# Performance work log

Hardware: AMD Instinct MI355X
Metric: run time of the kernel (lower is better)

Reference implementation:

```python
import jax, jax.numpy as jnp
import numpy as np

B, H, S, E = 1024, 64, 1, 512


def setup_inputs() -> dict:
    key = jax.random.key(0)
    k1, k2, k3, k4, k5 = jax.random.split(key, 5)
    return {
        "others1": jax.random.normal(k1, (B, H, S, E), dtype=jnp.float32),
        "others2": jax.random.normal(k2, (B, H, S, E), dtype=jnp.float32),
        "others3": jax.random.normal(k3, (B, H, S, E), dtype=jnp.float32),
        "main": jax.random.normal(k4, (B, H, S, E), dtype=jnp.float32),
        "W": jax.random.normal(k5, (E, E), dtype=jnp.float32) * 0.02,
    }


def reference(others1, others2, others3, main, W):
    # mean over the 'other' modalities, then drop the seq dim (squeeze(2))
    mean = (others1 + others2 + others3) / 3.0  # (B,H,1,E)
    m = mean[:, :, 0, :]   # (B,H,E)
    q = main[:, :, 0, :]   # (B,H,E)
    # score = mean @ W @ main^T  -> (B,H,H)
    score = jnp.einsum('bhe,ef,bgf->bhg', m, W, q)
    attn = jax.nn.softmax(score, axis=-1)          # (B,H,H)
    context = jnp.einsum('bhg,bge->bhe', attn, q)  # (B,H,E)
    return context, attn
```

## Files before the change

kernel.cpp:

```cpp
#include <hip/hip_runtime.h>
#include <hip/hip_bf16.h>

typedef _Float16 half4_t __attribute__((ext_vector_type(4)));
typedef _Float16 half8_t __attribute__((ext_vector_type(8)));
typedef float    float4_t __attribute__((ext_vector_type(4)));

#define MFMA32(a, b, c) __builtin_amdgcn_mfma_f32_16x16x32_f16((a), (b), (c), 0, 0, 0)

constexpr int  Bb  = 1024;
constexpr long CTX = (long)Bb * 64 * 512;
constexpr int  SQP = 520;
constexpr int  QTP = 72;

__global__ void w_pack(const float* __restrict__ W, _Float16* __restrict__ W2) {
    const int t = blockIdx.x * 256 + threadIdx.x;
    const int lane = t & 63, grp = t >> 6;
    const int E = grp >> 4, c = grp & 15;
    const int r16 = lane & 15, q = lane >> 4;
    const float* src = W + (long)(E * 16 + r16) * 512 + c * 32 + q * 8;
    float4_t x = *(const float4_t*)(src);
    float4_t y = *(const float4_t*)(src + 4);
    half8_t h;
    h[0]=(_Float16)x[0]; h[1]=(_Float16)x[1]; h[2]=(_Float16)x[2]; h[3]=(_Float16)x[3];
    h[4]=(_Float16)y[0]; h[5]=(_Float16)y[1]; h[6]=(_Float16)y[2]; h[7]=(_Float16)y[3];
    *(half8_t*)(W2 + (long)t * 8) = h;
}

__global__ __launch_bounds__(512, 4)
void ovo_score(const float* __restrict__ o1, const float* __restrict__ o2,
               const float* __restrict__ o3, const float* __restrict__ qm,
               const _Float16* __restrict__ W2, float* __restrict__ out)
{
    __shared__ __align__(16) _Float16 sQ[64 * SQP];

    const int t = threadIdx.x, lane = t & 63, w = t >> 6;
    const int r16 = lane & 15, q = lane >> 4;
    const long base = (long)blockIdx.x * 64 * 512;
    const float4_t zf4 = {0.f, 0.f, 0.f, 0.f};

    {
        const int srow = t >> 3;
        const int sf   = (t & 7) * 4;
        const float* qsrc = qm + base + (long)srow * 512 + sf;
        _Float16*    qdst = &sQ[srow * SQP + sf];
        #pragma unroll
        for (int k = 0; k < 16; ++k) {
            float4_t v = *(const float4_t*)(qsrc + k * 32);
            half4_t h;
            h[0]=(_Float16)v[0]; h[1]=(_Float16)v[1]; h[2]=(_Float16)v[2]; h[3]=(_Float16)v[3];
            *(half4_t*)(qdst + k * 32) = h;
        }
    }
    __syncthreads();

    float4_t vacc[4][4];
    #pragma unroll
    for (int i = 0; i < 4; ++i)
        #pragma unroll
        for (int j = 0; j < 4; ++j) vacc[i][j] = zf4;

    #pragma unroll
    for (int c = 0; c < 16; ++c) {
        half8_t Aq[4], Bw[4];
        #pragma unroll
        for (int gt = 0; gt < 4; ++gt)
            Aq[gt] = *(const half8_t*)(&sQ[(gt * 16 + r16) * SQP + c * 32 + q * 8]);
        #pragma unroll
        for (int et = 0; et < 4; ++et)
            Bw[et] = *(const half8_t*)(W2 + (long)((w * 4 + et) * 16 + c) * 512 + lane * 8);
        #pragma unroll
        for (int gt = 0; gt < 4; ++gt)
            #pragma unroll
            for (int et = 0; et < 4; ++et)
                vacc[gt][et] = MFMA32(Aq[gt], Bw[et], vacc[gt][et]);
    }

    __syncthreads();
    #pragma unroll
    for (int gt = 0; gt < 4; ++gt)
        #pragma unroll
        for (int et = 0; et < 4; ++et)
            #pragma unroll
            for (int r = 0; r < 4; ++r)
                sQ[(gt * 16 + q * 4 + r) * SQP + w * 64 + et * 16 + r16] =
                    (_Float16)vacc[gt][et][r];
    __syncthreads();

    const int ht = w & 3, eh = w >> 2;
    const long abase = base + (long)(ht * 16 + r16) * 512 + eh * 256 + q * 8;
    const int esV = eh * 256 + q * 8;

    float4_t sacc[4];
    #pragma unroll
    for (int i = 0; i < 4; ++i) sacc[i] = zf4;

    float4_t a1A, b1A, a2A, b2A, a3A, b3A;
    float4_t a1B, b1B, a2B, b2B, a3B, b3B;

    #define SLOAD(S, c) do { \
        const long o_ = abase + (c) * 32; \
        a1##S = *(const float4_t*)(o1 + o_); b1##S = *(const float4_t*)(o1 + o_ + 4); \
        a2##S = *(const float4_t*)(o2 + o_); b2##S = *(const float4_t*)(o2 + o_ + 4); \
        a3##S = *(const float4_t*)(o3 + o_); b3##S = *(const float4_t*)(o3 + o_ + 4); \
    } while (0)

    #define SCOMP(S, c) do { \
        float4_t m0 = (a1##S + a2##S + a3##S) * (1.0f / 3.0f); \
        float4_t m1 = (b1##S + b2##S + b3##S) * (1.0f / 3.0f); \
        half8_t af; \
        af[0]=(_Float16)m0[0]; af[1]=(_Float16)m0[1]; af[2]=(_Float16)m0[2]; af[3]=(_Float16)m0[3]; \
        af[4]=(_Float16)m1[0]; af[5]=(_Float16)m1[1]; af[6]=(_Float16)m1[2]; af[7]=(_Float16)m1[3]; \
        _Pragma("unroll") \
        for (int gt = 0; gt < 4; ++gt) { \
            half8_t bf = *(const half8_t*)(&sQ[(gt * 16 + r16) * SQP + esV + (c) * 32]); \
            sacc[gt] = MFMA32(af, bf, sacc[gt]); \
        } \
    } while (0)

    SLOAD(A, 0);
    #pragma unroll
    for (int cc = 0; cc < 8; cc += 2) {
        SLOAD(B, cc + 1);
        SCOMP(A, cc);
        if (cc + 2 < 8) SLOAD(A, cc + 2);
        SCOMP(B, cc + 1);
    }

    __syncthreads();
    float* part = reinterpret_cast<float*>(sQ);
    if (w >= 4) {
        #pragma unroll
        for (int gt = 0; gt < 4; ++gt)
            *(float4_t*)(&part[(((w - 4) * 4 + gt) * 64 + lane) * 4]) = sacc[gt];
    }
    __syncthreads();
    if (w < 4) {
        #pragma unroll
        for (int gt = 0; gt < 4; ++gt)
            sacc[gt] += *(const float4_t*)(&part[((w * 4 + gt) * 64 + lane) * 4]);
        #pragma unroll
        for (int r = 0; r < 4; ++r) {
            float mx = fmaxf(fmaxf(sacc[0][r], sacc[1][r]), fmaxf(sacc[2][r], sacc[3][r]));
            mx = fmaxf(mx, __shfl_xor(mx, 1));
            mx = fmaxf(mx, __shfl_xor(mx, 2));
            mx = fmaxf(mx, __shfl_xor(mx, 4));
            mx = fmaxf(mx, __shfl_xor(mx, 8));
            float p0 = __expf(sacc[0][r] - mx), p1 = __expf(sacc[1][r] - mx);
            float p2 = __expf(sacc[2][r] - mx), p3 = __expf(sacc[3][r] - mx);
            float s = p0 + p1 + p2 + p3;
            s += __shfl_xor(s, 1); s += __shfl_xor(s, 2);
            s += __shfl_xor(s, 4); s += __shfl_xor(s, 8);
            const float inv = 1.0f / s;
            float* arow = out + CTX + ((long)blockIdx.x * 64 + w * 16 + q * 4 + r) * 64;
            arow[ 0 + r16] = p0 * inv;
            arow[16 + r16] = p1 * inv;
            arow[32 + r16] = p2 * inv;
            arow[48 + r16] = p3 * inv;
        }
    }
}

__global__ __launch_bounds__(256, 4)
void ovo_ctx(const float* __restrict__ qm, const float* __restrict__ out_attn,
             float* __restrict__ out)
{
    __shared__ __align__(16) _Float16 qT[2][64 * QTP];

    const int t = threadIdx.x, lane = t & 63, w = t >> 6;
    const int r16 = lane & 15, q = lane >> 4;
    const long b = blockIdx.x;
    const long base = b * 64 * 512;
    const float4_t zf4 = {0.f, 0.f, 0.f, 0.f};

    const float* ap = out_attn + (b * 64 + w * 16 + r16) * 64 + q * 8;
    half8_t pA0, pA1;
    {
        float4_t x = *(const float4_t*)(ap + 0),  y = *(const float4_t*)(ap + 4);
        pA0[0]=(_Float16)x[0]; pA0[1]=(_Float16)x[1]; pA0[2]=(_Float16)x[2]; pA0[3]=(_Float16)x[3];
        pA0[4]=(_Float16)y[0]; pA0[5]=(_Float16)y[1]; pA0[6]=(_Float16)y[2]; pA0[7]=(_Float16)y[3];
        float4_t z = *(const float4_t*)(ap + 32), u = *(const float4_t*)(ap + 36);
        pA1[0]=(_Float16)z[0]; pA1[1]=(_Float16)z[1]; pA1[2]=(_Float16)z[2]; pA1[3]=(_Float16)z[3];
        pA1[4]=(_Float16)u[0]; pA1[5]=(_Float16)u[1]; pA1[6]=(_Float16)u[2]; pA1[7]=(_Float16)u[3];
    }

    const int sg = t & 63, se = (t >> 6) * 16;
    const float* qsrc = qm + base + (long)sg * 512 + se;
    float4_t rA[4], rB[4];

    #define QLOAD(R, c) do { \
        _Pragma("unroll") \
        for (int i = 0; i < 4; ++i) R[i] = *(const float4_t*)(qsrc + (c) * 64 + i * 4); \
    } while (0)
    #define QCOMMIT(R, buf) do { \
        _Pragma("unroll") \
        for (int i = 0; i < 4; ++i) \
            _Pragma("unroll") \
            for (int jj = 0; jj < 4; ++jj) \
                qT[buf][(se + i * 4 + jj) * QTP + sg] = (_Float16)R[i][jj]; \
    } while (0)

    #define BCOMP(c, buf) do { \
        _Pragma("unroll") \
        for (int et = 0; et < 4; ++et) { \
            half8_t b0 = *(const half8_t*)(&qT[buf][(et * 16 + r16) * QTP + q * 8]); \
            half8_t b1 = *(const half8_t*)(&qT[buf][(et * 16 + r16) * QTP + 32 + q * 8]); \
            float4_t acc = MFMA32(pA0, b0, zf4); \
            acc = MFMA32(pA1, b1, acc); \
            _Pragma("unroll") \
            for (int rr = 0; rr < 4; ++rr) \
                out[(b * 64 + w * 16 + q * 4 + rr) * 512 + (c) * 64 + et * 16 + r16] = acc[rr]; \
        } \
    } while (0)

    QLOAD(rA, 0);
    QCOMMIT(rA, 0);
    __syncthreads();
    #pragma unroll
    for (int cc = 0; cc < 8; cc += 2) {
        QLOAD(rB, cc + 1);
        BCOMP(cc, 0);
        QCOMMIT(rB, 1);
        __syncthreads();
        if (cc + 2 < 8) QLOAD(rA, cc + 2);
        BCOMP(cc + 1, 1);
        if (cc + 2 < 8) QCOMMIT(rA, 0);
        __syncthreads();
    }
}

extern "C" void kernel_launch(void* const* d_in, const int* in_sizes, int n_in,
                              void* d_out, int out_size, void* d_ws, size_t ws_size,
                              hipStream_t stream) {
    const float* o1 = (const float*)d_in[0];
    const float* o2 = (const float*)d_in[1];
    const float* o3 = (const float*)d_in[2];
    const float* qm = (const float*)d_in[3];
    const float* W  = (const float*)d_in[4];
    float* out = (float*)d_out;
    _Float16* W2 = (_Float16*)d_ws;

    w_pack<<<dim3(128), dim3(256), 0, stream>>>(W, W2);
    ovo_score<<<dim3(Bb), dim3(512), 0, stream>>>(o1, o2, o3, qm, W2, out);
    ovo_ctx<<<dim3(Bb), dim3(256), 0, stream>>>(qm, out + CTX, out);
}
```

Measured before the change: 211.6 us.

## Stage mean rows through double-buffered LDS with coalesced loads overlapping score MFMAs

The score kernel now loads the three 'other' tensors with fully coalesced contiguous float4 reads into registers, averages them and commits 16-row fp16 chunks into a double-buffered LDS tile (sM). Prefetch of the next chunk is overlapped with the MFMA work on the current chunk. The score tile is then staged through LDS so each softmax row can be handled with contiguous reads and vectorised row writes. This adds LDS usage and register pressure (launch bounds lowered to 2 blocks per CU), trading occupancy for better memory coalescing and overlap.

```diff
diff --git a/kernel.cpp b/kernel.cpp
--- a/kernel.cpp
+++ b/kernel.cpp
@@ -10,6 +10,8 @@
 constexpr int  Bb  = 1024;
 constexpr long CTX = (long)Bb * 64 * 512;
 constexpr int  SQP = 520;
+constexpr int  SMP = 520;
+constexpr int  SP  = 65;
 constexpr int  QTP = 72;
 
 __global__ void w_pack(const float* __restrict__ W, _Float16* __restrict__ W2) {
@@ -26,31 +28,47 @@
     *(half8_t*)(W2 + (long)t * 8) = h;
 }
 
-__global__ __launch_bounds__(512, 4)
+__global__ __launch_bounds__(512, 2)
 void ovo_score(const float* __restrict__ o1, const float* __restrict__ o2,
                const float* __restrict__ o3, const float* __restrict__ qm,
                const _Float16* __restrict__ W2, float* __restrict__ out)
 {
     __shared__ __align__(16) _Float16 sQ[64 * SQP];
+    __shared__ __align__(16) _Float16 sM[2][16 * SMP];
 
     const int t = threadIdx.x, lane = t & 63, w = t >> 6;
     const int r16 = lane & 15, q = lane >> 4;
+    const int gt = w & 3, eh = w >> 2;
     const long base = (long)blockIdx.x * 64 * 512;
     const float4_t zf4 = {0.f, 0.f, 0.f, 0.f};
 
+    float4_t rA[12], rB[12];
+    #define OLOAD(R, hc) do { \
+        const long fb = base + (long)(hc) * 8192 + (long)t * 4; \
+        _Pragma("unroll") for (int i = 0; i < 4; ++i) R[i]     = *(const float4_t*)(o1 + fb + i * 2048); \
+        _Pragma("unroll") for (int i = 0; i < 4; ++i) R[4 + i] = *(const float4_t*)(o2 + fb + i * 2048); \
+        _Pragma("unroll") for (int i = 0; i < 4; ++i) R[8 + i] = *(const float4_t*)(o3 + fb + i * 2048); \
+    } while (0)
+    #define OCOMMIT(R, buf) do { \
+        _Pragma("unroll") for (int i = 0; i < 4; ++i) { \
+            float4_t m = (R[i] + R[4 + i] + R[8 + i]) * (1.0f / 3.0f); \
+            half4_t h; \
+            h[0]=(_Float16)m[0]; h[1]=(_Float16)m[1]; h[2]=(_Float16)m[2]; h[3]=(_Float16)m[3]; \
+            *(half4_t*)(&sM[buf][(i * 4 + (t >> 7)) * SMP + (t & 127) * 4]) = h; \
+        } \
+    } while (0)
+
     {
-        const int srow = t >> 3;
-        const int sf   = (t & 7) * 4;
-        const float* qsrc = qm + base + (long)srow * 512 + sf;
-        _Float16*    qdst = &sQ[srow * SQP + sf];
+        const long qb = base + (long)t * 4;
         #pragma unroll
         for (int k = 0; k < 16; ++k) {
-            float4_t v = *(const float4_t*)(qsrc + k * 32);
+            float4_t v = *(const float4_t*)(qm + qb + (long)k * 2048);
             half4_t h;
             h[0]=(_Float16)v[0]; h[1]=(_Float16)v[1]; h[2]=(_Float16)v[2]; h[3]=(_Float16)v[3];
-            *(half4_t*)(qdst + k * 32) = h;
+            *(half4_t*)(&sQ[(k * 4 + (t >> 7)) * SQP + (t & 127) * 4]) = h;
         }
     }
+    OLOAD(rA, 0);
     __syncthreads();
 
     float4_t vacc[4][4];
@@ -63,100 +81,93 @@
     for (int c = 0; c < 16; ++c) {
         half8_t Aq[4], Bw[4];
         #pragma unroll
-        for (int gt = 0; gt < 4; ++gt)
-            Aq[gt] = *(const half8_t*)(&sQ[(gt * 16 + r16) * SQP + c * 32 + q * 8]);
+        for (int g2 = 0; g2 < 4; ++g2)
+            Aq[g2] = *(const half8_t*)(&sQ[(g2 * 16 + r16) * SQP + c * 32 + q * 8]);
         #pragma unroll
         for (int et = 0; et < 4; ++et)
             Bw[et] = *(const half8_t*)(W2 + (long)((w * 4 + et) * 16 + c) * 512 + lane * 8);
         #pragma unroll
-        for (int gt = 0; gt < 4; ++gt)
+        for (int g2 = 0; g2 < 4; ++g2)
             #pragma unroll
             for (int et = 0; et < 4; ++et)
-                vacc[gt][et] = MFMA32(Aq[gt], Bw[et], vacc[gt][et]);
-    }
-
-    __syncthreads();
-    #pragma unroll
-    for (int gt = 0; gt < 4; ++gt)
+                vacc[g2][et] = MFMA32(Aq[g2], Bw[et], vacc[g2][et]);
+    }
+    __syncthreads();
+
+    #pragma unroll
+    for (int g2 = 0; g2 < 4; ++g2)
         #pragma unroll
         for (int et = 0; et < 4; ++et)
             #pragma unroll
             for (int r = 0; r < 4; ++r)
-                sQ[(gt * 16 + q * 4 + r) * SQP + w * 64 + et * 16 + r16] =
-                    (_Float16)vacc[gt][et][r];
-    __syncthreads();
-
-    const int ht = w & 3, eh = w >> 2;
-    const long abase = base + (long)(ht * 16 + r16) * 512 + eh * 256 + q * 8;
-    const int esV = eh * 256 + q * 8;
-
-    float4_t sacc[4];
-    #pragma unroll
-    for (int i = 0; i < 4; ++i) sacc[i] = zf4;
-
-    float4_t a1A, b1A, a2A, b2A, a3A, b3A;
-    float4_t a1B, b1B, a2B, b2B, a3B, b3B;
-
-    #define SLOAD(S, c) do { \
-        const long o_ = abase + (c) * 32; \
-        a1##S = *(const float4_t*)(o1 + o_); b1##S = *(const float4_t*)(o1 + o_ + 4); \
-        a2##S = *(const float4_t*)(o2 + o_); b2##S = *(const float4_t*)(o2 + o_ + 4); \
-        a3##S = *(const float4_t*)(o3 + o_); b3##S = *(const float4_t*)(o3 + o_ + 4); \
-    } while (0)
-
-    #define SCOMP(S, c) do { \
-        float4_t m0 = (a1##S + a2##S + a3##S) * (1.0f / 3.0f); \
-        float4_t m1 = (b1##S + b2##S + b3##S) * (1.0f / 3.0f); \
-        half8_t af; \
-        af[0]=(_Float16)m0[0]; af[1]=(_Float16)m0[1]; af[2]=(_Float16)m0[2]; af[3]=(_Float16)m0[3]; \
-        af[4]=(_Float16)m1[0]; af[5]=(_Float16)m1[1]; af[6]=(_Float16)m1[2]; af[7]=(_Float16)m1[3]; \
-        _Pragma("unroll") \
-        for (int gt = 0; gt < 4; ++gt) { \
-            half8_t bf = *(const half8_t*)(&sQ[(gt * 16 + r16) * SQP + esV + (c) * 32]); \
-            sacc[gt] = MFMA32(af, bf, sacc[gt]); \
+                sQ[(g2 * 16 + q * 4 + r) * SQP + w * 64 + et * 16 + r16] =
+                    (_Float16)vacc[g2][et][r];
+    OCOMMIT(rA, 0);
+    OLOAD(rB, 1);
+    __syncthreads();
+
+    float4_t acc0 = zf4, acc1 = zf4, acc2 = zf4, acc3 = zf4;
+    #define SCHUNK(ACC, buf) do { \
+        _Pragma("unroll") for (int c = 0; c < 8; ++c) { \
+            const int cc = eh * 8 + c; \
+            half8_t af = *(const half8_t*)(&sM[buf][r16 * SMP + cc * 32 + q * 8]); \
+            half8_t bf = *(const half8_t*)(&sQ[(gt * 16 + r16) * SQP + cc * 32 + q * 8]); \
+            ACC = MFMA32(af, bf, ACC); \
         } \
     } while (0)
 
-    SLOAD(A, 0);
-    #pragma unroll
-    for (int cc = 0; cc < 8; cc += 2) {
-        SLOAD(B, cc + 1);
-        SCOMP(A, cc);
-        if (cc + 2 < 8) SLOAD(A, cc + 2);
-        SCOMP(B, cc + 1);
-    }
-
-    __syncthreads();
-    float* part = reinterpret_cast<float*>(sQ);
-    if (w >= 4) {
-        #pragma unroll
-        for (int gt = 0; gt < 4; ++gt)
-            *(float4_t*)(&part[(((w - 4) * 4 + gt) * 64 + lane) * 4]) = sacc[gt];
-    }
-    __syncthreads();
+    SCHUNK(acc0, 0); OCOMMIT(rB, 1); OLOAD(rA, 2);
+    __syncthreads();
+    SCHUNK(acc1, 1); OCOMMIT(rA, 0); OLOAD(rB, 3);
+    __syncthreads();
+    SCHUNK(acc2, 0); OCOMMIT(rB, 1);
+    __syncthreads();
+    SCHUNK(acc3, 1);
+    __syncthreads();
+
+    float4_t* part4 = reinterpret_cast<float4_t*>(&sM[0][0]);
+    float*    sS    = reinterpret_cast<float*>(&sQ[0]);
+    if (eh == 1) {
+        part4[(gt * 4 + 0) * 64 + lane] = acc0;
+        part4[(gt * 4 + 1) * 64 + lane] = acc1;
+        part4[(gt * 4 + 2) * 64 + lane] = acc2;
+        part4[(gt * 4 + 3) * 64 + lane] = acc3;
+    }
+    __syncthreads();
+    if (eh == 0) {
+        acc0 += part4[(gt * 4 + 0) * 64 + lane];
+        acc1 += part4[(gt * 4 + 1) * 64 + lane];
+        acc2 += part4[(gt * 4 + 2) * 64 + lane];
+        acc3 += part4[(gt * 4 + 3) * 64 + lane];
+        #pragma unroll
+        for (int r = 0; r < 4; ++r) {
+            sS[( 0 + q * 4 + r) * SP + gt * 16 + r16] = acc0[r];
+            sS[(16 + q * 4 + r) * SP + gt * 16 + r16] = acc1[r];
+            sS[(32 + q * 4 + r) * SP + gt * 16 + r16] = acc2[r];
+            sS[(48 + q * 4 + r) * SP + gt * 16 + r16] = acc3[r];
+        }
+    }
+    __syncthreads();
+
     if (w < 4) {
-        #pragma unroll
-        for (int gt = 0; gt < 4; ++gt)
-            sacc[gt] += *(const float4_t*)(&part[((w * 4 + gt) * 64 + lane) * 4]);
-        #pragma unroll
-        for (int r = 0; r < 4; ++r) {
-            float mx = fmaxf(fmaxf(sacc[0][r], sacc[1][r]), fmaxf(sacc[2][r], sacc[3][r]));
-            mx = fmaxf(mx, __shfl_xor(mx, 1));
-            mx = fmaxf(mx, __shfl_xor(mx, 2));
-            mx = fmaxf(mx, __shfl_xor(mx, 4));
-            mx = fmaxf(mx, __shfl_xor(mx, 8));
-            float p0 = __expf(sacc[0][r] - mx), p1 = __expf(sacc[1][r] - mx);
-            float p2 = __expf(sacc[2][r] - mx), p3 = __expf(sacc[3][r] - mx);
-            float s = p0 + p1 + p2 + p3;
-            s += __shfl_xor(s, 1); s += __shfl_xor(s, 2);
-            s += __shfl_xor(s, 4); s += __shfl_xor(s, 8);
-            const float inv = 1.0f / s;
-            float* arow = out + CTX + ((long)blockIdx.x * 64 + w * 16 + q * 4 + r) * 64;
-            arow[ 0 + r16] = p0 * inv;
-            arow[16 + r16] = p1 * inv;
-            arow[32 + r16] = p2 * inv;
-            arow[48 + r16] = p3 * inv;
-        }
+        const int r  = w * 16 + r16;
+        const int qd = lane >> 4;
+        const float* srow = sS + r * SP + qd * 16;
+        float v[16];
+        float mx = -1e30f;
+        #pragma unroll
+        for (int i = 0; i < 16; ++i) { v[i] = srow[i]; mx = fmaxf(mx, v[i]); }
+        mx = fmaxf(mx, __shfl_xor(mx, 16));
+        mx = fmaxf(mx, __shfl_xor(mx, 32));
+        float sum = 0.f;
+        #pragma unroll
+        for (int i = 0; i < 16; ++i) { v[i] = __expf(v[i] - mx); sum += v[i]; }
+        sum += __shfl_xor(sum, 16);
+        sum += __shfl_xor(sum, 32);
+        const float inv = 1.0f / sum;
+        float* aout = out + CTX + ((long)blockIdx.x * 64 + r) * 64 + qd * 16;
+        #pragma unroll
+        for (int i = 0; i < 16; ++i) aout[i] = v[i] * inv;
     }
 }
 
@@ -198,7 +209,6 @@
             for (int jj = 0; jj < 4; ++jj) \
                 qT[buf][(se + i * 4 + jj) * QTP + sg] = (_Float16)R[i][jj]; \
     } while (0)
-
     #define BCOMP(c, buf) do { \
         _Pragma("unroll") \
         for (int et = 0; et < 4; ++et) { \
```

Result: faster. 198.7 us (-6.1%).
